# Kernel tuning notes

Measured on AMD Instinct MI355X. Metric: run time of the kernel, lower is better.

## Reference

```python
import jax, jax.numpy as jnp
import numpy as np

N = 100000
E = 1600000
F_IN = 32
F_OUT = 32


def setup_inputs() -> dict:
    key = jax.random.key(0)
    ks = jax.random.split(key, 12)
    x = jax.random.normal(ks[0], (N, F_IN), jnp.float32)
    edge_index = jax.random.randint(ks[1], (2, E), 0, N)
    edge_weight = jax.random.uniform(ks[2], (E,), jnp.float32)
    s = 0.1
    return {
        "x": x,
        "edge_index": edge_index,
        "edge_weight": edge_weight,
        "Wz": jax.random.normal(ks[3], (F_IN, F_OUT), jnp.float32) * s,
        "bz": jnp.zeros((F_OUT,), jnp.float32),
        "Wr": jax.random.normal(ks[4], (F_IN, F_OUT), jnp.float32) * s,
        "br": jnp.zeros((F_OUT,), jnp.float32),
        "Wh": jax.random.normal(ks[5], (F_IN, F_OUT), jnp.float32) * s,
        "bh": jnp.zeros((F_OUT,), jnp.float32),
        "Lz_W": jax.random.normal(ks[6], (2 * F_OUT, F_OUT), jnp.float32) * s,
        "Lz_b": jnp.zeros((F_OUT,), jnp.float32),
        "Lr_W": jax.random.normal(ks[7], (2 * F_OUT, F_OUT), jnp.float32) * s,
        "Lr_b": jnp.zeros((F_OUT,), jnp.float32),
        "Lh_W": jax.random.normal(ks[8], (2 * F_OUT, F_OUT), jnp.float32) * s,
        "Lh_b": jnp.zeros((F_OUT,), jnp.float32),
        "lin_W": jax.random.normal(ks[9], (F_OUT, 1), jnp.float32) * s,
        "lin_b": jnp.zeros((1,), jnp.float32),
    }


def reference(x, edge_index, edge_weight, Wz, bz, Wr, br, Wh, bh,
              Lz_W, Lz_b, Lr_W, Lr_b, Lh_W, Lh_b, lin_W, lin_b):
    n = x.shape[0]
    f_out = Wz.shape[1]
    row, col = edge_index[0], edge_index[1]
    # GCN normalization with added self-loops (PyG gcn_norm, improved=False)
    loop = jnp.arange(n, dtype=row.dtype)
    row_ = jnp.concatenate([row, loop])
    col_ = jnp.concatenate([col, loop])
    ew = jnp.concatenate([edge_weight, jnp.ones((n,), edge_weight.dtype)])
    deg = jax.ops.segment_sum(ew, col_, num_segments=n)
    dinv = jnp.where(deg > 0, jax.lax.rsqrt(deg), 0.0)
    norm = dinv[row_] * ew * dinv[col_]  # [E+N]

    def conv(W, b):
        xw = x @ W                                   # [N, f_out]
        msg = xw[row_] * norm[:, None]               # gather + scale [E+N, f_out]
        return jax.ops.segment_sum(msg, col_, num_segments=n) + b

    H = jnp.zeros((n, f_out), x.dtype)  # TGCN default hidden state
    Z = jax.nn.sigmoid(jnp.concatenate([conv(Wz, bz), H], axis=1) @ Lz_W + Lz_b)
    R = jax.nn.sigmoid(jnp.concatenate([conv(Wr, br), H], axis=1) @ Lr_W + Lr_b)
    H_tilde = jnp.tanh(jnp.concatenate([conv(Wh, bh), H * R], axis=1) @ Lh_W + Lh_b)
    H = Z * H + (1.0 - Z) * H_tilde
    h = jax.nn.relu(H)
    return h @ lin_W + lin_b
```

## Files before the change

kernel.cpp:

```cpp
#include <hip/hip_runtime.h>
#include <hip/hip_fp16.h>
#include <math.h>

#define F 32
#define FC 64
#define MAXDEG 64
#define BINSHIFT 9
#define BINW 512
#define CHUNKS 128

__device__ inline float h15_to_f(unsigned v) {
  __half_raw hr; hr.x = (unsigned short)(v & 0x7FFFu);
  return __half2float(*reinterpret_cast<__half*>(&hr));
}

__global__ void k_p1(const int* __restrict__ ei, int e_total, int chsz, int nb,
                     int* __restrict__ histM,
                     const float* __restrict__ Wz, const float* __restrict__ Wh,
                     const float* __restrict__ LzW, const float* __restrict__ LhW,
                     const float* __restrict__ bz, const float* __restrict__ bh,
                     const float* __restrict__ Lzb, const float* __restrict__ Lhb,
                     float* __restrict__ Mcomb, float* __restrict__ czh) {
  if ((int)blockIdx.x < CHUNKS) {
    __shared__ int hist[256];
    hist[threadIdx.x] = 0;
    __syncthreads();
    int k = blockIdx.x;
    int lo = k * chsz;
    int hi = lo + chsz; if (hi > e_total) hi = e_total;
    for (int e = lo + threadIdx.x; e < hi; e += 256)
      atomicAdd(&hist[ei[e_total + e] >> BINSHIFT], 1);
    __syncthreads();
    int t = threadIdx.x;
    if (t < nb) histM[t * CHUNKS + k] = hist[t];
    return;
  }
  int t = threadIdx.x;
  for (int idx = t; idx < F * FC; idx += blockDim.x) {
    int k = idx / FC, j = idx % FC;
    float s = 0.f;
    if (j < F) { for (int m = 0; m < F; ++m) s = fmaf(Wz[k*F+m], LzW[m*F+j], s); }
    else { int jj = j-F; for (int m = 0; m < F; ++m) s = fmaf(Wh[k*F+m], LhW[m*F+jj], s); }
    Mcomb[idx] = s;
  }
  if (t < FC) {
    float s;
    if (t < F) { s = Lzb[t]; for (int k = 0; k < F; ++k) s = fmaf(bz[k], LzW[k*F+t], s); }
    else { int jj = t-F; s = Lhb[jj]; for (int k = 0; k < F; ++k) s = fmaf(bh[k], LhW[k*F+jj], s); }
    czh[t] = s;
  }
}

__global__ void k_p2a(const int* __restrict__ histM, int* __restrict__ chunkOff,
                      int* __restrict__ colsum, int nb) {
  __shared__ int s[2][CHUNKS];
  int b = blockIdx.x, k = threadIdx.x;
  int h = histM[b * CHUNKS + k];
  s[0][k] = h;
  __syncthreads();
  int src = 0;
  for (int d = 1; d < CHUNKS; d <<= 1) {
    int v = s[src][k];
    if (k >= d) v += s[src][k - d];
    s[src ^ 1][k] = v; src ^= 1;
    __syncthreads();
  }
  int incl = s[src][k];
  chunkOff[k * nb + b] = incl - h;
  if (k == CHUNKS - 1) colsum[b] = incl;
}

__global__ void k_p2b(const int* __restrict__ colsum, int* __restrict__ binStart,
                      int nb, int e_total) {
  __shared__ int s[2][256];
  int t = threadIdx.x;
  int v = (t < nb) ? colsum[t] : 0;
  s[0][t] = v;
  __syncthreads();
  int src = 0;
  for (int d = 1; d < 256; d <<= 1) {
    int x = s[src][t];
    if (t >= d) x += s[src][t - d];
    s[src ^ 1][t] = x; src ^= 1;
    __syncthreads();
  }
  if (t < nb) binStart[t] = s[src][t] - v;
  if (t == 0) binStart[nb] = e_total;
}

__global__ void k_p3(const int* __restrict__ ei, const float* __restrict__ ew,
                     const int* __restrict__ chunkOff, const int* __restrict__ binStart,
                     uint2* __restrict__ part, int e_total, int chsz, int nb) {
  __shared__ int cursor[256];
  int k = blockIdx.x, t = threadIdx.x;
  if (t < nb) cursor[t] = chunkOff[k * nb + t] + binStart[t];
  __syncthreads();
  int lo = k * chsz;
  int hi = lo + chsz; if (hi > e_total) hi = e_total;
  for (int e = lo + t; e < hi; e += 256) {
    int r = ei[e];
    int c = ei[e_total + e];
    float w = ew[e];
    int b = c >> BINSHIFT;
    int pos = atomicAdd(&cursor[b], 1);
    uint2 v;
    v.x = ((unsigned)(c & (BINW - 1)) << 17) | (unsigned)r;
    v.y = __float_as_uint(w);
    part[pos] = v;
  }
}

__global__ void k_p4(const uint2* __restrict__ part, const int* __restrict__ binStart,
                     unsigned* __restrict__ pk, unsigned long long* __restrict__ deg64,
                     int n) {
  __shared__ unsigned long long dg[BINW];
  int b = blockIdx.x, t = threadIdx.x;
  for (int u = t; u < BINW; u += 256) dg[u] = 0ull;
  __syncthreads();
  int lo = binStart[b], hi = binStart[b + 1];
  for (int e = lo + t; e < hi; e += 256) {
    uint2 v = part[e];
    unsigned r  = v.x & 0x1FFFFu;
    unsigned cl = v.x >> 17;
    float w = __uint_as_float(v.y);
    unsigned long long fx = (unsigned long long)((double)w * 4294967296.0) + (1ull << 48);
    unsigned long long old = atomicAdd(&dg[cl], fx);
    unsigned rank = (unsigned)(old >> 48);
    if (rank < MAXDEG) {
      unsigned hv = (unsigned)__half_as_ushort(__float2half(w)) & 0x7FFFu;
      unsigned c = ((unsigned)b << BINSHIFT) | cl;
      pk[((size_t)c << 6) | rank] = (r << 15) | hv;
    }
  }
  __syncthreads();
  int base = b << BINSHIFT;
  for (int u = t; u < BINW; u += 256) {
    int i = base + u;
    if (i < n) deg64[i] = dg[u];
  }
}

__global__ void k_xw(const float* __restrict__ x, const float* __restrict__ Mcomb,
                     const unsigned long long* __restrict__ deg64,
                     __half* __restrict__ XWs, int n) {
  __shared__ float M[F * FC];
  __shared__ float xt[32][F];
  int t = threadIdx.x;
  for (int u = t; u < F * FC; u += 256) M[u] = Mcomb[u];
  int tile = blockIdx.x << 5;
  {
    int node = t >> 3;
    if (tile + node < n)
      ((float4*)xt)[t] = ((const float4*)(x + (size_t)tile * F))[t];
  }
  __syncthreads();
  int j = t & 63;
  int g = t >> 6;
  float mcol[F];
#pragma unroll
  for (int k = 0; k < F; ++k) mcol[k] = M[k * FC + j];
#pragma unroll
  for (int u = 0; u < 8; ++u) {
    int node = (g << 3) + u;
    int i = tile + node;
    if (i >= n) break;
    float acc = 0.f;
#pragma unroll
    for (int k = 0; k < F; ++k) acc = fmaf(xt[node][k], mcol[k], acc);
    unsigned long long dv = deg64[i];
    float s = 1.0f + (float)((double)(dv & 0xFFFFFFFFFFFFull) * (1.0 / 4294967296.0));
    float di = rsqrtf(s);
    XWs[((size_t)i << 6) | j] = __float2half(di * acc);
  }
}

__global__ void k_agg(const __half2* __restrict__ XW2,
                      const unsigned long long* __restrict__ deg64,
                      const unsigned* __restrict__ pk,
                      const float* __restrict__ czh,
                      const float* __restrict__ linW, const float* __restrict__ linb,
                      float* __restrict__ out, int n) {
  int wid = (blockIdx.x * blockDim.x + threadIdx.x) >> 6;
  int j = threadIdx.x & 63;
  if (wid >= n) return;
  int hj = j & 31, hh = j >> 5;
  unsigned long long dv = deg64[wid];
  int cnt = (int)(dv >> 48);
  cnt = (cnt > MAXDEG) ? MAXDEG : cnt;
  float s = 1.0f + (float)((double)(dv & 0xFFFFFFFFFFFFull) * (1.0 / 4294967296.0));
  float di = rsqrtf(s);
  unsigned pv = pk[((size_t)wid << 6) | j];
  float2 a0 = make_float2(0.f, 0.f), a1 = make_float2(0.f, 0.f);
  if (hh == 0) {
    float2 sp = __half22float2(XW2[((size_t)wid << 5) + hj]);
    a0.x = sp.x; a0.y = sp.y;
  }
  int e = 0;
  for (; e + 4 <= cnt; e += 4) {
    unsigned v0 = __shfl(pv, e + hh, 64);
    unsigned v1 = __shfl(pv, e + 2 + hh, 64);
    float2 f0 = __half22float2(XW2[((size_t)(v0 >> 15) << 5) + hj]);
    float2 f1 = __half22float2(XW2[((size_t)(v1 >> 15) << 5) + hj]);
    float w0 = h15_to_f(v0), w1 = h15_to_f(v1);
    a0.x = fmaf(w0, f0.x, a0.x); a0.y = fmaf(w0, f0.y, a0.y);
    a1.x = fmaf(w1, f1.x, a1.x); a1.y = fmaf(w1, f1.y, a1.y);
  }
  for (; e < cnt; e += 2) {
    int src = e + hh;
    int sl = (src < cnt) ? src : (cnt - 1);
    unsigned v = __shfl(pv, sl, 64);
    if (src < cnt) {
      float2 f = __half22float2(XW2[((size_t)(v >> 15) << 5) + hj]);
      float w = h15_to_f(v);
      a0.x = fmaf(w, f.x, a0.x); a0.y = fmaf(w, f.y, a0.y);
    }
  }
  float2 acc = make_float2(a0.x + a1.x, a0.y + a1.y);
  acc.x += __shfl_xor(acc.x, 32, 64);
  acc.y += __shfl_xor(acc.y, 32, 64);
  float2 cz = ((const float2*)czh)[hj];
  float ax = fmaf(acc.x, di, cz.x);
  float ay = fmaf(acc.y, di, cz.y);
  float gx, gy;
  if (hj < 16) { gx = 1.f / (1.f + expf(-ax)); gy = 1.f / (1.f + expf(-ay)); }
  else         { gx = tanhf(ax); gy = tanhf(ay); }
  float ox = __shfl_xor(gx, 16, 64);
  float oy = __shfl_xor(gy, 16, 64);
  float val = 0.f;
  if (hh == 0 && hj < 16) {
    float hnx = (1.f - gx) * ox;
    float hny = (1.f - gy) * oy;
    float2 lw = ((const float2*)linW)[hj];
    val = fmaxf(hnx, 0.f) * lw.x + fmaxf(hny, 0.f) * lw.y;
  }
#pragma unroll
  for (int d = 32; d > 0; d >>= 1) val += __shfl_xor(val, d, 64);
  if (j == 0) out[wid] = val + linb[0];
}

extern "C" void kernel_launch(void* const* d_in, const int* in_sizes, int n_in,
                              void* d_out, int out_size, void* d_ws, size_t ws_size,
                              hipStream_t stream) {
  const float* x   = (const float*)d_in[0];
  const int*   ei  = (const int*)d_in[1];
  const float* ew  = (const float*)d_in[2];
  const float* Wz  = (const float*)d_in[3];
  const float* bz  = (const float*)d_in[4];
  const float* Wh  = (const float*)d_in[7];
  const float* bh  = (const float*)d_in[8];
  const float* LzW = (const float*)d_in[9];
  const float* Lzb = (const float*)d_in[10];
  const float* LhW = (const float*)d_in[13];
  const float* Lhb = (const float*)d_in[14];
  const float* lnW = (const float*)d_in[15];
  const float* lnb = (const float*)d_in[16];
  float* out = (float*)d_out;

  const int n = in_sizes[0] / F;
  const int e_total = in_sizes[2];
  const int nb = (n + BINW - 1) >> BINSHIFT;
  const int chsz = (e_total + CHUNKS - 1) / CHUNKS;

  char* p = (char*)d_ws;
  auto alloc = [&](size_t bytes) -> void* {
    void* q = (void*)p;
    p += (bytes + 255) & ~(size_t)255;
    return q;
  };
  float* Mcomb  = (float*)alloc((size_t)F * FC * 4);
  float* czh    = (float*)alloc(FC * 4);
  unsigned long long* deg64 = (unsigned long long*)alloc((size_t)n * 8);
  int* histM    = (int*)alloc((size_t)CHUNKS * nb * 4);
  int* chunkOff = (int*)alloc((size_t)CHUNKS * nb * 4);
  int* colsum   = (int*)alloc((size_t)nb * 4);
  int* binStart = (int*)alloc(((size_t)nb + 1) * 4);
  uint2* part   = (uint2*)alloc((size_t)e_total * 8);
  unsigned* pk  = (unsigned*)alloc(((size_t)n << 6) * 4);
  __half* XWs   = (__half*)part;

  dim3 blk(256);
  int nxblocks = (n + 31) >> 5;
  int wblocks = (int)(((size_t)n * 64 + 255) / 256);

  k_p1<<<CHUNKS + 1, blk, 0, stream>>>(ei, e_total, chsz, nb, histM,
      Wz, Wh, LzW, LhW, bz, bh, Lzb, Lhb, Mcomb, czh);
  k_p2a<<<nb, CHUNKS, 0, stream>>>(histM, chunkOff, colsum, nb);
  k_p2b<<<1, blk, 0, stream>>>(colsum, binStart, nb, e_total);
  k_p3<<<CHUNKS, blk, 0, stream>>>(ei, ew, chunkOff, binStart, part, e_total, chsz, nb);
  k_p4<<<nb, blk, 0, stream>>>(part, binStart, pk, deg64, n);
  k_xw<<<nxblocks, blk, 0, stream>>>(x, Mcomb, deg64, XWs, n);
  k_agg<<<wblocks, blk, 0, stream>>>((const __half2*)XWs, deg64, pk, czh, lnW, lnb, out, n);
}
```

Before: 130.3 us.

## Gather neighbor rows with 16-byte loads, 8 edges per wave step

The aggregation kernel now splits each 64-lane wave into 8 groups of 8 lanes. Each lane loads 16 bytes (8 halves) of a neighbor's 64-wide fp16 row, so one wave processes 8 edges per iteration instead of 2. A cross-group shuffle reduction combines the partial sums before the gate math. This cuts load instruction count and loop iterations per node, at the cost of more shuffles and wasted lanes when a node has few edges. The number of sort chunks is also doubled to 256 to spread the histogram and scatter work across more blocks.

```diff
diff --git a/kernel.cpp b/kernel.cpp
--- a/kernel.cpp
+++ b/kernel.cpp
@@ -7,11 +7,15 @@
 #define MAXDEG 64
 #define BINSHIFT 9
 #define BINW 512
-#define CHUNKS 128
+#define CHUNKS 256
 
 __device__ inline float h15_to_f(unsigned v) {
   __half_raw hr; hr.x = (unsigned short)(v & 0x7FFFu);
   return __half2float(*reinterpret_cast<__half*>(&hr));
+}
+__device__ inline float2 h2f2(unsigned u) {
+  __half2 h = *reinterpret_cast<__half2*>(&u);
+  return __half22float2(h);
 }
 
 __global__ void k_p1(const int* __restrict__ ei, int e_total, int chsz, int nb,
@@ -174,7 +178,7 @@
   }
 }
 
-__global__ void k_agg(const __half2* __restrict__ XW2,
+__global__ void k_agg(const __half* __restrict__ XWs,
                       const unsigned long long* __restrict__ deg64,
                       const unsigned* __restrict__ pk,
                       const float* __restrict__ czh,
@@ -183,55 +187,70 @@
   int wid = (blockIdx.x * blockDim.x + threadIdx.x) >> 6;
   int j = threadIdx.x & 63;
   if (wid >= n) return;
-  int hj = j & 31, hh = j >> 5;
+  int g = j >> 3, c = j & 7;
   unsigned long long dv = deg64[wid];
   int cnt = (int)(dv >> 48);
   cnt = (cnt > MAXDEG) ? MAXDEG : cnt;
   float s = 1.0f + (float)((double)(dv & 0xFFFFFFFFFFFFull) * (1.0 / 4294967296.0));
   float di = rsqrtf(s);
   unsigned pv = pk[((size_t)wid << 6) | j];
-  float2 a0 = make_float2(0.f, 0.f), a1 = make_float2(0.f, 0.f);
-  if (hh == 0) {
-    float2 sp = __half22float2(XW2[((size_t)wid << 5) + hj]);
-    a0.x = sp.x; a0.y = sp.y;
-  }
-  int e = 0;
-  for (; e + 4 <= cnt; e += 4) {
-    unsigned v0 = __shfl(pv, e + hh, 64);
-    unsigned v1 = __shfl(pv, e + 2 + hh, 64);
-    float2 f0 = __half22float2(XW2[((size_t)(v0 >> 15) << 5) + hj]);
-    float2 f1 = __half22float2(XW2[((size_t)(v1 >> 15) << 5) + hj]);
-    float w0 = h15_to_f(v0), w1 = h15_to_f(v1);
-    a0.x = fmaf(w0, f0.x, a0.x); a0.y = fmaf(w0, f0.y, a0.y);
-    a1.x = fmaf(w1, f1.x, a1.x); a1.y = fmaf(w1, f1.y, a1.y);
-  }
-  for (; e < cnt; e += 2) {
-    int src = e + hh;
-    int sl = (src < cnt) ? src : (cnt - 1);
-    unsigned v = __shfl(pv, sl, 64);
-    if (src < cnt) {
-      float2 f = __half22float2(XW2[((size_t)(v >> 15) << 5) + hj]);
-      float w = h15_to_f(v);
-      a0.x = fmaf(w, f.x, a0.x); a0.y = fmaf(w, f.y, a0.y);
+  float acc[8];
+#pragma unroll
+  for (int k = 0; k < 8; ++k) acc[k] = 0.f;
+  if (g == 0) {
+    uint4 d = *((const uint4*)(XWs + ((size_t)wid << 6)) + c);
+    float2 p0 = h2f2(d.x), p1 = h2f2(d.y), p2 = h2f2(d.z), p3 = h2f2(d.w);
+    acc[0] = p0.x; acc[1] = p0.y; acc[2] = p1.x; acc[3] = p1.y;
+    acc[4] = p2.x; acc[5] = p2.y; acc[6] = p3.x; acc[7] = p3.y;
+  }
+  for (int e = 0; e < cnt; e += 8) {
+    int slot = e + g;
+    unsigned v = __shfl(pv, slot, 64);
+    bool valid = slot < cnt;
+    float w = valid ? h15_to_f(v) : 0.f;
+    unsigned row = valid ? (v >> 15) : 0u;
+    uint4 d = *((const uint4*)(XWs + ((size_t)row << 6)) + c);
+    float2 p0 = h2f2(d.x), p1 = h2f2(d.y), p2 = h2f2(d.z), p3 = h2f2(d.w);
+    acc[0] = fmaf(w, p0.x, acc[0]); acc[1] = fmaf(w, p0.y, acc[1]);
+    acc[2] = fmaf(w, p1.x, acc[2]); acc[3] = fmaf(w, p1.y, acc[3]);
+    acc[4] = fmaf(w, p2.x, acc[4]); acc[5] = fmaf(w, p2.y, acc[5]);
+    acc[6] = fmaf(w, p3.x, acc[6]); acc[7] = fmaf(w, p3.y, acc[7]);
+  }
+#pragma unroll
+  for (int mask = 8; mask <= 32; mask <<= 1)
+#pragma unroll
+    for (int k = 0; k < 8; ++k)
+      acc[k] += __shfl_xor(acc[k], mask, 64);
+  float val = 0.f;
+  if (g == 0) {
+    float4 cz0 = ((const float4*)czh)[2 * c];
+    float4 cz1 = ((const float4*)czh)[2 * c + 1];
+    float a[8];
+    a[0] = fmaf(acc[0], di, cz0.x); a[1] = fmaf(acc[1], di, cz0.y);
+    a[2] = fmaf(acc[2], di, cz0.z); a[3] = fmaf(acc[3], di, cz0.w);
+    a[4] = fmaf(acc[4], di, cz1.x); a[5] = fmaf(acc[5], di, cz1.y);
+    a[6] = fmaf(acc[6], di, cz1.z); a[7] = fmaf(acc[7], di, cz1.w);
+    float gv[8];
+    if (c < 4) {
+#pragma unroll
+      for (int k = 0; k < 8; ++k) gv[k] = 1.f / (1.f + expf(-a[k]));
+    } else {
+#pragma unroll
+      for (int k = 0; k < 8; ++k) gv[k] = tanhf(a[k]);
     }
-  }
-  float2 acc = make_float2(a0.x + a1.x, a0.y + a1.y);
-  acc.x += __shfl_xor(acc.x, 32, 64);
-  acc.y += __shfl_xor(acc.y, 32, 64);
-  float2 cz = ((const float2*)czh)[hj];
-  float ax = fmaf(acc.x, di, cz.x);
-  float ay = fmaf(acc.y, di, cz.y);
-  float gx, gy;
-  if (hj < 16) { gx = 1.f / (1.f + expf(-ax)); gy = 1.f / (1.f + expf(-ay)); }
-  else         { gx = tanhf(ax); gy = tanhf(ay); }
-  float ox = __shfl_xor(gx, 16, 64);
-  float oy = __shfl_xor(gy, 16, 64);
-  float val = 0.f;
-  if (hh == 0 && hj < 16) {
-    float hnx = (1.f - gx) * ox;
-    float hny = (1.f - gy) * oy;
-    float2 lw = ((const float2*)linW)[hj];
-    val = fmaxf(hnx, 0.f) * lw.x + fmaxf(hny, 0.f) * lw.y;
+    float ov[8];
+#pragma unroll
+    for (int k = 0; k < 8; ++k) ov[k] = __shfl_xor(gv[k], 4, 64);
+    if (c < 4) {
+      float4 lw0 = ((const float4*)linW)[2 * c];
+      float4 lw1 = ((const float4*)linW)[2 * c + 1];
+      float lw[8] = {lw0.x, lw0.y, lw0.z, lw0.w, lw1.x, lw1.y, lw1.z, lw1.w};
+#pragma unroll
+      for (int k = 0; k < 8; ++k) {
+        float hn = (1.f - gv[k]) * ov[k];
+        val = fmaf(fmaxf(hn, 0.f), lw[k], val);
+      }
+    }
   }
 #pragma unroll
   for (int d = 32; d > 0; d >>= 1) val += __shfl_xor(val, d, 64);
@@ -289,5 +308,5 @@
   k_p3<<<CHUNKS, blk, 0, stream>>>(ei, ew, chunkOff, binStart, part, e_total, chsz, nb);
   k_p4<<<nb, blk, 0, stream>>>(part, binStart, pk, deg64, n);
   k_xw<<<nxblocks, blk, 0, stream>>>(x, Mcomb, deg64, XWs, n);
-  k_agg<<<wblocks, blk, 0, stream>>>((const __half2*)XWs, deg64, pk, czh, lnW, lnb, out, n);
-}
+  k_agg<<<wblocks, blk, 0, stream>>>(XWs, deg64, pk, czh, lnW, lnb, out, n);
+}
```

Measured after the change: 140.8 us. 8.1% more time.
